# Kernel optimization log

Measured on AMD Instinct MI355X. Metric: run time of the kernel, lower is better.

Reference implementation:

```python
import jax, jax.numpy as jnp
import numpy as np

E = 512
H = 8
D = E // H  # head_dim = 64
SCALE = D ** -0.5
NEG_INF = float('-inf')


def layer_norm(x, g, b, eps=1e-5):
    mu = jnp.mean(x, axis=-1, keepdims=True)
    var = jnp.var(x, axis=-1, keepdims=True)
    return (x - mu) * jax.lax.rsqrt(var + eps) * g + b


def setup_inputs() -> dict:
    key = jax.random.key(0)
    ks = jax.random.split(key, 16)
    B, Q, K = 4, 2048, 2048
    inp = {
        'query': jax.random.normal(ks[0], (B, Q, E), jnp.float32),
        'key_value': jax.random.normal(ks[1], (B, K, E), jnp.float32),
        'kv_mask': jax.random.randint(ks[2], (B, K), 0, 2) > 0,
        'sparse_mask': jax.random.randint(ks[3], (B, Q, K), 0, 2) > 0,
        'ln_q_g': jnp.ones((E,), jnp.float32),
        'ln_q_b': jnp.zeros((E,), jnp.float32),
        'ln_kv_g': jnp.ones((E,), jnp.float32),
        'ln_kv_b': jnp.zeros((E,), jnp.float32),
        # Linear weights stored as (in, out): y = x @ W + b
        'Wq': jax.random.normal(ks[4], (E, E), jnp.float32) * (E ** -0.5),
        'bq': jnp.zeros((E,), jnp.float32),
        'Wk': jax.random.normal(ks[5], (E, E), jnp.float32) * (E ** -0.5),
        'bk': jnp.zeros((E,), jnp.float32),
        'Wv': jax.random.normal(ks[6], (E, E), jnp.float32) * (E ** -0.5),
        'bv': jnp.zeros((E,), jnp.float32),
        'Wo': jax.random.normal(ks[7], (E, E), jnp.float32) * (E ** -0.5),
        'bo': jnp.zeros((E,), jnp.float32),
    }
    return inp


def reference(query, key_value, kv_mask, sparse_mask,
              ln_q_g, ln_q_b, ln_kv_g, ln_kv_b,
              Wq, bq, Wk, bk, Wv, bv, Wo, bo):
    B, Qn, _ = query.shape
    Kn = key_value.shape[1]
    qn = layer_norm(query, ln_q_g, ln_q_b)
    kvn = layer_norm(key_value, ln_kv_g, ln_kv_b)
    q = (qn @ Wq + bq).reshape(B, Qn, H, D)
    k = (kvn @ Wk + bk).reshape(B, Kn, H, D)
    v = (kvn @ Wv + bv).reshape(B, Kn, H, D)
    # scores: [B, H, Q, K]
    scores = jnp.einsum('bqhd,bkhd->bhqk', q, k) * SCALE
    mask = kv_mask[:, None, None, :] & sparse_mask[:, None, :, :]
    scores = jnp.where(mask, scores, NEG_INF)
    attn = jax.nn.softmax(scores, axis=-1)
    # nan_to_num(0): rows with no valid key -> all-zero weights
    valid_row = jnp.any(mask, axis=-1, keepdims=True)
    attn = jnp.where(valid_row, attn, 0.0)
    out = jnp.einsum('bhqk,bkhd->bqhd', attn, v).reshape(B, Qn, E)
    return out @ Wo + bo
```

## Files before the change

### kernel.cpp

```cpp
#include <hip/hip_runtime.h>
#include <hip/hip_bf16.h>
#include <math.h>

typedef unsigned short ushort_t;
typedef __attribute__((ext_vector_type(8))) __bf16 bf16x8;
typedef __attribute__((ext_vector_type(4))) float f32x4;
typedef __attribute__((ext_vector_type(4))) unsigned int u32x4;

#define E_DIM 512
#define HEADS 8
#define HD 64
#define SEQ 2048
#define NROWS 8192
#define QSCALE 0.18033688011112042f

static __device__ __forceinline__ unsigned short f2b(float f) {
  unsigned int x;
  __builtin_memcpy(&x, &f, 4);
  x += 0x7fffu + ((x >> 16) & 1u);
  return (unsigned short)(x >> 16);
}

static __device__ __forceinline__ int swz(int row, int col) {
  return row * 64 + ((((col >> 3) ^ (row & 7)) & 7) << 3) + (col & 7);
}

static __device__ __forceinline__ void gl2lds16(const ushort_t* g, ushort_t* s) {
#if __has_builtin(__builtin_amdgcn_global_load_lds)
  __builtin_amdgcn_global_load_lds(
      (const __attribute__((address_space(1))) unsigned int*)(uintptr_t)g,
      (__attribute__((address_space(3))) unsigned int*)(uintptr_t)s,
      16, 0, 0);
#else
  int l = threadIdx.x & 63;
  *(u32x4*)(s + l * 8) = *(const u32x4*)g;
#endif
}

__launch_bounds__(256)
__global__ void prep_kernel(const float* __restrict__ Wq, const float* __restrict__ Wk,
                            const float* __restrict__ Wv, const float* __restrict__ Wo,
                            ushort_t* __restrict__ WT,
                            const int* __restrict__ kvm, const int* __restrict__ sp,
                            unsigned long long* __restrict__ bits,
                            const float* __restrict__ xq, const float* __restrict__ xkv,
                            const float* __restrict__ gq, const float* __restrict__ bq,
                            const float* __restrict__ gkv, const float* __restrict__ bkv,
                            ushort_t* __restrict__ yq, ushort_t* __restrict__ ykv) {
  int blk = blockIdx.x;
  int t = threadIdx.x;
  if (blk < 1024) {
    int z = blk >> 8, rem = blk & 255;
    const float* in = (z == 0) ? Wq : (z == 1) ? Wk : (z == 2) ? Wv : Wo;
    ushort_t* o = WT + (size_t)z * E_DIM * E_DIM;
    __shared__ float tile[32 * 33];
    int tx = t & 31, ty = t >> 5;
    int n0 = (rem & 15) * 32, k0 = (rem >> 4) * 32;
#pragma unroll
    for (int i = 0; i < 4; ++i) {
      int k = ty + i * 8;
      tile[k * 33 + tx] = in[(k0 + k) * E_DIM + n0 + tx];
    }
    __syncthreads();
#pragma unroll
    for (int i = 0; i < 4; ++i) {
      int n = ty + i * 8;
      o[(n0 + n) * E_DIM + k0 + tx] = f2b(tile[tx * 33 + n]);
    }
  } else if (blk < 3072) {
    int w = t >> 6, l = t & 63;
    int row = (blk - 1024) * 4 + w;
    int b = row >> 11;
    const int* sprow = sp + ((size_t)row << 11);
    const int* kvrow = kvm + (b << 11);
    unsigned long long* out = bits + ((size_t)row << 5);
#pragma unroll 4
    for (int it = 0; it < 32; ++it) {
      int k = it * 64 + l;
      unsigned long long m = __ballot(sprow[k] != 0 && kvrow[k] != 0);
      if (l == 0) out[it] = m;
    }
  } else {
    int idx = blk - 3072;
    int which = idx >> 11;
    const float* x = which ? xkv : xq;
    const float* g = which ? gkv : gq;
    const float* bb = which ? bkv : bq;
    ushort_t* y = which ? ykv : yq;
    int w = t >> 6, l = t & 63;
    int row = (idx & 2047) * 4 + w;
    f32x4 x0 = *(const f32x4*)&x[row * E_DIM + l * 8];
    f32x4 x1 = *(const f32x4*)&x[row * E_DIM + l * 8 + 4];
    float xf[8], s = 0.f, ss = 0.f;
#pragma unroll
    for (int j = 0; j < 8; ++j) {
      xf[j] = (j < 4) ? x0[j] : x1[j - 4];
      s += xf[j];
      ss += xf[j] * xf[j];
    }
#pragma unroll
    for (int off = 32; off > 0; off >>= 1) {
      s += __shfl_xor(s, off);
      ss += __shfl_xor(ss, off);
    }
    float mu = s * (1.f / 512.f);
    float var = fmaxf(ss * (1.f / 512.f) - mu * mu, 0.f);
    float rs = rsqrtf(var + 1e-5f);
    f32x4 g0 = *(const f32x4*)&g[l * 8];
    f32x4 g1 = *(const f32x4*)&g[l * 8 + 4];
    f32x4 b0 = *(const f32x4*)&bb[l * 8];
    f32x4 b1 = *(const f32x4*)&bb[l * 8 + 4];
#pragma unroll
    for (int j = 0; j < 8; ++j) {
      float gv = (j < 4) ? g0[j] : g1[j - 4];
      float bv = (j < 4) ? b0[j] : b1[j - 4];
      y[row * E_DIM + l * 8 + j] = f2b((xf[j] - mu) * rs * gv + bv);
    }
  }
}

__launch_bounds__(256)
__global__ void transposeV(const ushort_t* __restrict__ vp, ushort_t* __restrict__ Vt) {
  __shared__ ushort_t tile[64][72];
  int t = threadIdx.x;
  int k0 = blockIdx.x * 64, h = blockIdx.y, b = blockIdx.z;
#pragma unroll
  for (int it = 0; it < 2; ++it) {
    int row = it * 32 + (t >> 3), col = (t & 7) * 8;
    *(u32x4*)&tile[row][col] =
        *(const u32x4*)&vp[(size_t)(b * SEQ + k0 + row) * E_DIM + h * HD + col];
  }
  __syncthreads();
#pragma unroll
  for (int it = 0; it < 2; ++it) {
    int d = it * 32 + (t >> 3), kc = (t & 7) * 8;
    union { ushort_t u[8]; u32x4 v; } o;
#pragma unroll
    for (int j = 0; j < 8; ++j) o.u[j] = tile[kc + j][d];
    *(u32x4*)&Vt[((size_t)(b * HEADS + h) * HD + d) * SEQ + k0 + kc] = o.v;
  }
}

template <typename OUT_T>
static __device__ __forceinline__ void gemm_core(ushort_t* lA, ushort_t* lB,
                                                 const ushort_t* __restrict__ A,
                                                 const ushort_t* __restrict__ WT,
                                                 const float* __restrict__ bias,
                                                 OUT_T* __restrict__ C, float scale,
                                                 int m0, int n0) {
  int t = threadIdx.x, w = t >> 6, l = t & 63;
  int quad = l >> 4, l15 = l & 15;
  int wm_ = w >> 1, wn_ = w & 1;
  int csrc = ((l & 7) ^ (l >> 3)) * 8;
  int rln = l >> 3;

  f32x4 acc[4][2] = {};
  for (int kk = 0; kk < E_DIM; kk += 64) {
    __syncthreads();
#pragma unroll
    for (int i = 0; i < 4; ++i) {
      int r0 = i * 32 + w * 8;
      gl2lds16(&A[(size_t)(m0 + r0 + rln) * E_DIM + kk + csrc], &lA[r0 * 64]);
    }
#pragma unroll
    for (int i = 0; i < 2; ++i) {
      int r0 = i * 32 + w * 8;
      gl2lds16(&WT[(size_t)(n0 + r0 + rln) * E_DIM + kk + csrc], &lB[r0 * 64]);
    }
    __syncthreads();
#pragma unroll
    for (int ks = 0; ks < 2; ++ks) {
      bf16x8 af[4], bf[2];
#pragma unroll
      for (int mt = 0; mt < 4; ++mt)
        af[mt] = *(const bf16x8*)&lA[swz(wm_ * 64 + mt * 16 + l15, ks * 32 + quad * 8)];
#pragma unroll
      for (int nt = 0; nt < 2; ++nt)
        bf[nt] = *(const bf16x8*)&lB[swz(wn_ * 32 + nt * 16 + l15, ks * 32 + quad * 8)];
#pragma unroll
      for (int mt = 0; mt < 4; ++mt)
#pragma unroll
        for (int nt = 0; nt < 2; ++nt)
          acc[mt][nt] = __builtin_amdgcn_mfma_f32_16x16x32_bf16(af[mt], bf[nt], acc[mt][nt], 0, 0, 0);
    }
  }
#pragma unroll
  for (int nt = 0; nt < 2; ++nt) {
    int col = n0 + wn_ * 32 + nt * 16 + l15;
    float bv = bias[col];
#pragma unroll
    for (int mt = 0; mt < 4; ++mt) {
#pragma unroll
      for (int r = 0; r < 4; ++r) {
        int rowm = m0 + wm_ * 64 + mt * 16 + quad * 4 + r;
        float val = (acc[mt][nt][r] + bv) * scale;
        if constexpr (sizeof(OUT_T) == 2)
          C[rowm * E_DIM + col] = f2b(val);
        else
          C[rowm * E_DIM + col] = val;
      }
    }
  }
}

template <typename OUT_T>
__launch_bounds__(256)
__global__ void gemm_bias(const ushort_t* __restrict__ A, const ushort_t* __restrict__ WT,
                          const float* __restrict__ bias, OUT_T* __restrict__ C, float scale) {
  __shared__ ushort_t lA[128 * 64];
  __shared__ ushort_t lB[64 * 64];
  gemm_core<OUT_T>(lA, lB, A, WT, bias, C, scale, blockIdx.x * 128, blockIdx.y * 64);
}

__launch_bounds__(256)
__global__ void gemm_proj2(const ushort_t* A0, const ushort_t* W0, const float* b0, ushort_t* C0, float s0,
                           const ushort_t* A1, const ushort_t* W1, const float* b1, ushort_t* C1, float s1) {
  __shared__ ushort_t lA[128 * 64];
  __shared__ ushort_t lB[64 * 64];
  int m0 = blockIdx.x * 128, n0 = blockIdx.y * 64;
  if (blockIdx.z == 0) gemm_core<ushort_t>(lA, lB, A0, W0, b0, C0, s0, m0, n0);
  else                 gemm_core<ushort_t>(lA, lB, A1, W1, b1, C1, s1, m0, n0);
}

__launch_bounds__(256)
__global__ void attn_kernel(const ushort_t* __restrict__ Qp, const ushort_t* __restrict__ Kp,
                            const ushort_t* __restrict__ Vt,
                            const unsigned long long* __restrict__ bits,
                            ushort_t* __restrict__ ctx) {
  __shared__ ushort_t sQ[64 * 64];
  __shared__ ushort_t sK[64 * 64];
  __shared__ ushort_t sVt[64 * 64];
  __shared__ ushort_t sP[64 * 64];
  int t = threadIdx.x, w = t >> 6, l = t & 63;
  int quad = l >> 4, l15 = l & 15;
  int q0 = blockIdx.x * 64;
  int h = blockIdx.y;
  int b = blockIdx.z;
  int bh = b * HEADS + h;
  int myq = w * 16 + l15;
  int csrc = ((l & 7) ^ (l >> 3)) * 8;
  int rln = l >> 3;

#pragma unroll
  for (int it = 0; it < 2; ++it) {
    int r0 = it * 32 + w * 8;
    gl2lds16(&Qp[(size_t)(b * SEQ + q0 + r0 + rln) * E_DIM + h * HD + csrc], &sQ[r0 * 64]);
  }

  const unsigned long long* mrow = bits + ((size_t)(b * SEQ + q0 + myq) << 5);
  float lsum = 0.f;
  f32x4 o[4] = {};

  for (int kt = 0; kt < 32; ++kt) {
    int k0 = kt * 64;
    __syncthreads();
#pragma unroll
    for (int it = 0; it < 2; ++it) {
      int r0 = it * 32 + w * 8;
      gl2lds16(&Kp[(size_t)(b * SEQ + k0 + r0 + rln) * E_DIM + h * HD + csrc], &sK[r0 * 64]);
      gl2lds16(&Vt[((size_t)bh * HD + r0 + rln) * SEQ + k0 + csrc], &sVt[r0 * 64]);
    }
    __syncthreads();

    f32x4 s[4] = {};
#pragma unroll
    for (int ks = 0; ks < 2; ++ks) {
      bf16x8 qf = *(const bf16x8*)&sQ[swz(myq, ks * 32 + quad * 8)];
#pragma unroll
      for (int nt = 0; nt < 4; ++nt) {
        bf16x8 kf = *(const bf16x8*)&sK[swz(nt * 16 + l15, ks * 32 + quad * 8)];
        s[nt] = __builtin_amdgcn_mfma_f32_16x16x32_bf16(kf, qf, s[nt], 0, 0, 0);
      }
    }

    unsigned long long wmask = mrow[kt];
    unsigned sx = ((unsigned)wmask) >> (quad * 4);
    unsigned sy = ((unsigned)(wmask >> 32)) >> (quad * 4);
#pragma unroll
    for (int nt = 0; nt < 4; ++nt) {
      unsigned wsel = (nt & 2) ? sy : sx;
      int sh = (nt & 1) ? 16 : 0;
      union { ushort_t u[4]; uint2 v; } pk;
#pragma unroll
      for (int r = 0; r < 4; ++r) {
        float pv = exp2f(s[nt][r]);
        unsigned short uu = (unsigned short)(__float_as_uint(pv) >> 16);
        if (!((wsel >> (sh + r)) & 1u)) uu = 0;
        pk.u[r] = uu;
        lsum += __uint_as_float(((unsigned)uu) << 16);
      }
      *(uint2*)&sP[swz(myq, nt * 16 + quad * 4)] = pk.v;
    }

#pragma unroll
    for (int ks = 0; ks < 2; ++ks) {
      bf16x8 pf = *(const bf16x8*)&sP[swz(myq, ks * 32 + quad * 8)];
#pragma unroll
      for (int mt = 0; mt < 4; ++mt) {
        bf16x8 vf = *(const bf16x8*)&sVt[swz(mt * 16 + l15, ks * 32 + quad * 8)];
        o[mt] = __builtin_amdgcn_mfma_f32_16x16x32_bf16(vf, pf, o[mt], 0, 0, 0);
      }
    }
  }

  lsum += __shfl_xor(lsum, 16);
  lsum += __shfl_xor(lsum, 32);
  float inv = (lsum > 0.f) ? 1.f / lsum : 0.f;
  size_t base = (size_t)(b * SEQ + q0 + myq) * E_DIM + h * HD;
#pragma unroll
  for (int mt = 0; mt < 4; ++mt) {
    union { ushort_t u[4]; uint2 v; } ov;
#pragma unroll
    for (int r = 0; r < 4; ++r) ov.u[r] = f2b(o[mt][r] * inv);
    *(uint2*)&ctx[base + mt * 16 + quad * 4] = ov.v;
  }
}

extern "C" void kernel_launch(void* const* d_in, const int* in_sizes, int n_in,
                              void* d_out, int out_size, void* d_ws, size_t ws_size,
                              hipStream_t stream) {
  const float* query     = (const float*)d_in[0];
  const float* key_value = (const float*)d_in[1];
  const int*   kv_mask   = (const int*)d_in[2];
  const int*   sp_mask   = (const int*)d_in[3];
  const float* ln_q_g  = (const float*)d_in[4];
  const float* ln_q_b  = (const float*)d_in[5];
  const float* ln_kv_g = (const float*)d_in[6];
  const float* ln_kv_b = (const float*)d_in[7];
  const float* Wq = (const float*)d_in[8];
  const float* bq = (const float*)d_in[9];
  const float* Wk = (const float*)d_in[10];
  const float* bk = (const float*)d_in[11];
  const float* Wv = (const float*)d_in[12];
  const float* bv = (const float*)d_in[13];
  const float* Wo = (const float*)d_in[14];
  const float* bo = (const float*)d_in[15];

  const size_t NB = (size_t)NROWS * E_DIM;
  char* ws = (char*)d_ws;
  ushort_t* bufA = (ushort_t*)ws;
  ushort_t* bufB = bufA + NB;
  ushort_t* WT   = bufB + NB;
  ushort_t* WTq = WT;
  ushort_t* WTk = WTq + E_DIM * E_DIM;
  ushort_t* WTv = WTk + E_DIM * E_DIM;
  ushort_t* WTo = WTv + E_DIM * E_DIM;
  unsigned long long* bits = (unsigned long long*)(WTo + E_DIM * E_DIM);

  ushort_t* dlo = (ushort_t*)d_out;
  ushort_t* dhi = dlo + NB;

  prep_kernel<<<7168, 256, 0, stream>>>(Wq, Wk, Wv, Wo, WT, kv_mask, sp_mask, bits,
                                        query, key_value, ln_q_g, ln_q_b, ln_kv_g, ln_kv_b,
                                        dlo, bufA);

  gemm_proj2<<<dim3(64, 8, 2), 256, 0, stream>>>(dlo, WTq, bq, dhi, QSCALE,
                                                 bufA, WTv, bv, bufB, 1.f);

  gemm_bias<ushort_t><<<dim3(64, 8), 256, 0, stream>>>(bufA, WTk, bk, dlo, 1.f);

  transposeV<<<dim3(32, HEADS, 4), 256, 0, stream>>>(bufB, bufA);

  attn_kernel<<<dim3(32, HEADS, 4), 256, 0, stream>>>(dhi, dlo, bufA, bits, bufB);

  gemm_bias<float><<<dim3(64, 8), 256, 0, stream>>>(bufB, WTo, bo, (float*)d_out, 1.f);
}
```

Measured before the change: 295.8 us.

## Fuse V transpose into projection epilogue and widen GEMM tiles to 128x128

The V projection now writes its output directly in the head-transposed layout from the GEMM epilogue, so the separate transposeV kernel and its extra read and write pass are gone. All projection GEMMs move from 128x64 to 128x128 tiles (4x4 MFMA accumulators per wave), which halves the grid and raises data reuse per block. The attention softmax also changes to mask by substituting a large negative value before exp2 and to sum the fp32 probabilities instead of the truncated bf16 ones. The trade-offs are higher register use per thread, fewer blocks to fill the GPU, and strided 8-byte stores in the transposed epilogue.

New measurement: 289.5 us. 2.1% less time.

```diff
diff --git a/kernel.cpp b/kernel.cpp
--- a/kernel.cpp
+++ b/kernel.cpp
@@ -12,6 +12,7 @@
 #define HD 64
 #define SEQ 2048
 #define NROWS 8192
+#define NEGF (-1e30f)
 #define QSCALE 0.18033688011112042f
 
 static __device__ __forceinline__ unsigned short f2b(float f) {
@@ -119,107 +120,103 @@
   }
 }
 
-__launch_bounds__(256)
-__global__ void transposeV(const ushort_t* __restrict__ vp, ushort_t* __restrict__ Vt) {
-  __shared__ ushort_t tile[64][72];
-  int t = threadIdx.x;
-  int k0 = blockIdx.x * 64, h = blockIdx.y, b = blockIdx.z;
-#pragma unroll
-  for (int it = 0; it < 2; ++it) {
-    int row = it * 32 + (t >> 3), col = (t & 7) * 8;
-    *(u32x4*)&tile[row][col] =
-        *(const u32x4*)&vp[(size_t)(b * SEQ + k0 + row) * E_DIM + h * HD + col];
-  }
-  __syncthreads();
-#pragma unroll
-  for (int it = 0; it < 2; ++it) {
-    int d = it * 32 + (t >> 3), kc = (t & 7) * 8;
-    union { ushort_t u[8]; u32x4 v; } o;
-#pragma unroll
-    for (int j = 0; j < 8; ++j) o.u[j] = tile[kc + j][d];
-    *(u32x4*)&Vt[((size_t)(b * HEADS + h) * HD + d) * SEQ + k0 + kc] = o.v;
-  }
-}
-
-template <typename OUT_T>
-static __device__ __forceinline__ void gemm_core(ushort_t* lA, ushort_t* lB,
-                                                 const ushort_t* __restrict__ A,
-                                                 const ushort_t* __restrict__ WT,
-                                                 const float* __restrict__ bias,
-                                                 OUT_T* __restrict__ C, float scale,
-                                                 int m0, int n0) {
+template <int MODE>
+static __device__ __forceinline__ void gemm_core128(ushort_t* lA, ushort_t* lB,
+                                                    const ushort_t* __restrict__ A,
+                                                    const ushort_t* __restrict__ WT,
+                                                    const float* __restrict__ bias,
+                                                    void* Cv, float scale, int m0, int n0) {
   int t = threadIdx.x, w = t >> 6, l = t & 63;
   int quad = l >> 4, l15 = l & 15;
   int wm_ = w >> 1, wn_ = w & 1;
   int csrc = ((l & 7) ^ (l >> 3)) * 8;
   int rln = l >> 3;
 
-  f32x4 acc[4][2] = {};
+  f32x4 acc[4][4] = {};
   for (int kk = 0; kk < E_DIM; kk += 64) {
     __syncthreads();
 #pragma unroll
     for (int i = 0; i < 4; ++i) {
       int r0 = i * 32 + w * 8;
       gl2lds16(&A[(size_t)(m0 + r0 + rln) * E_DIM + kk + csrc], &lA[r0 * 64]);
-    }
-#pragma unroll
-    for (int i = 0; i < 2; ++i) {
-      int r0 = i * 32 + w * 8;
       gl2lds16(&WT[(size_t)(n0 + r0 + rln) * E_DIM + kk + csrc], &lB[r0 * 64]);
     }
     __syncthreads();
 #pragma unroll
     for (int ks = 0; ks < 2; ++ks) {
-      bf16x8 af[4], bf[2];
+      bf16x8 af[4], bf[4];
 #pragma unroll
       for (int mt = 0; mt < 4; ++mt)
         af[mt] = *(const bf16x8*)&lA[swz(wm_ * 64 + mt * 16 + l15, ks * 32 + quad * 8)];
 #pragma unroll
-      for (int nt = 0; nt < 2; ++nt)
-        bf[nt] = *(const bf16x8*)&lB[swz(wn_ * 32 + nt * 16 + l15, ks * 32 + quad * 8)];
+      for (int nt = 0; nt < 4; ++nt)
+        bf[nt] = *(const bf16x8*)&lB[swz(wn_ * 64 + nt * 16 + l15, ks * 32 + quad * 8)];
 #pragma unroll
       for (int mt = 0; mt < 4; ++mt)
 #pragma unroll
-        for (int nt = 0; nt < 2; ++nt)
+        for (int nt = 0; nt < 4; ++nt)
           acc[mt][nt] = __builtin_amdgcn_mfma_f32_16x16x32_bf16(af[mt], bf[nt], acc[mt][nt], 0, 0, 0);
     }
   }
-#pragma unroll
-  for (int nt = 0; nt < 2; ++nt) {
-    int col = n0 + wn_ * 32 + nt * 16 + l15;
+
+#pragma unroll
+  for (int nt = 0; nt < 4; ++nt) {
+    int col = n0 + wn_ * 64 + nt * 16 + l15;
     float bv = bias[col];
-#pragma unroll
-    for (int mt = 0; mt < 4; ++mt) {
-#pragma unroll
-      for (int r = 0; r < 4; ++r) {
-        int rowm = m0 + wm_ * 64 + mt * 16 + quad * 4 + r;
-        float val = (acc[mt][nt][r] + bv) * scale;
-        if constexpr (sizeof(OUT_T) == 2)
-          C[rowm * E_DIM + col] = f2b(val);
-        else
-          C[rowm * E_DIM + col] = val;
-      }
-    }
-  }
-}
-
-template <typename OUT_T>
-__launch_bounds__(256)
-__global__ void gemm_bias(const ushort_t* __restrict__ A, const ushort_t* __restrict__ WT,
-                          const float* __restrict__ bias, OUT_T* __restrict__ C, float scale) {
+    if constexpr (MODE == 2) {
+      int h = col >> 6, d = col & 63;
+#pragma unroll
+      for (int mt = 0; mt < 4; ++mt) {
+        int row = m0 + wm_ * 64 + mt * 16 + quad * 4;
+        int b = row >> 11, k = row & 2047;
+        union { ushort_t u[4]; uint2 v; } pk;
+#pragma unroll
+        for (int r = 0; r < 4; ++r) pk.u[r] = f2b(acc[mt][nt][r] + bv);
+        *(uint2*)&((ushort_t*)Cv)[((((size_t)(b * HEADS + h)) * HD + d) << 11) + k] = pk.v;
+      }
+    } else {
+#pragma unroll
+      for (int mt = 0; mt < 4; ++mt) {
+#pragma unroll
+        for (int r = 0; r < 4; ++r) {
+          int rowm = m0 + wm_ * 64 + mt * 16 + quad * 4 + r;
+          float val = (acc[mt][nt][r] + bv) * scale;
+          if constexpr (MODE == 0)
+            ((ushort_t*)Cv)[rowm * E_DIM + col] = f2b(val);
+          else
+            ((float*)Cv)[rowm * E_DIM + col] = val;
+        }
+      }
+    }
+  }
+}
+
+__launch_bounds__(256)
+__global__ void gemm128_bf16(const ushort_t* __restrict__ A, const ushort_t* __restrict__ WT,
+                             const float* __restrict__ bias, ushort_t* __restrict__ C, float scale) {
   __shared__ ushort_t lA[128 * 64];
-  __shared__ ushort_t lB[64 * 64];
-  gemm_core<OUT_T>(lA, lB, A, WT, bias, C, scale, blockIdx.x * 128, blockIdx.y * 64);
-}
-
-__launch_bounds__(256)
-__global__ void gemm_proj2(const ushort_t* A0, const ushort_t* W0, const float* b0, ushort_t* C0, float s0,
-                           const ushort_t* A1, const ushort_t* W1, const float* b1, ushort_t* C1, float s1) {
+  __shared__ ushort_t lB[128 * 64];
+  gemm_core128<0>(lA, lB, A, WT, bias, C, scale, blockIdx.x * 128, blockIdx.y * 128);
+}
+
+__launch_bounds__(256)
+__global__ void gemm128_f32(const ushort_t* __restrict__ A, const ushort_t* __restrict__ WT,
+                            const float* __restrict__ bias, float* __restrict__ C) {
   __shared__ ushort_t lA[128 * 64];
-  __shared__ ushort_t lB[64 * 64];
-  int m0 = blockIdx.x * 128, n0 = blockIdx.y * 64;
-  if (blockIdx.z == 0) gemm_core<ushort_t>(lA, lB, A0, W0, b0, C0, s0, m0, n0);
-  else                 gemm_core<ushort_t>(lA, lB, A1, W1, b1, C1, s1, m0, n0);
+  __shared__ ushort_t lB[128 * 64];
+  gemm_core128<1>(lA, lB, A, WT, bias, C, 1.f, blockIdx.x * 128, blockIdx.y * 128);
+}
+
+__launch_bounds__(256)
+__global__ void proj2_kernel(const ushort_t* __restrict__ qn, const ushort_t* __restrict__ WTq,
+                             const float* __restrict__ bq, ushort_t* __restrict__ qp,
+                             const ushort_t* __restrict__ kvn, const ushort_t* __restrict__ WTv,
+                             const float* __restrict__ bv, ushort_t* __restrict__ Vt) {
+  __shared__ ushort_t lA[128 * 64];
+  __shared__ ushort_t lB[128 * 64];
+  int m0 = blockIdx.x * 128, n0 = blockIdx.y * 128;
+  if (blockIdx.z == 0) gemm_core128<0>(lA, lB, qn, WTq, bq, qp, QSCALE, m0, n0);
+  else                 gemm_core128<2>(lA, lB, kvn, WTv, bv, Vt, 1.f, m0, n0);
 }
 
 __launch_bounds__(256)
@@ -283,11 +280,10 @@
       union { ushort_t u[4]; uint2 v; } pk;
 #pragma unroll
       for (int r = 0; r < 4; ++r) {
-        float pv = exp2f(s[nt][r]);
-        unsigned short uu = (unsigned short)(__float_as_uint(pv) >> 16);
-        if (!((wsel >> (sh + r)) & 1u)) uu = 0;
-        pk.u[r] = uu;
-        lsum += __uint_as_float(((unsigned)uu) << 16);
+        float smv = ((wsel >> (sh + r)) & 1u) ? s[nt][r] : NEGF;
+        float pv = exp2f(smv);
+        pk.u[r] = (unsigned short)(__float_as_uint(pv) >> 16);
+        lsum += pv;
       }
       *(uint2*)&sP[swz(myq, nt * 16 + quad * 4)] = pk.v;
     }
@@ -354,14 +350,12 @@
                                         query, key_value, ln_q_g, ln_q_b, ln_kv_g, ln_kv_b,
                                         dlo, bufA);
 
-  gemm_proj2<<<dim3(64, 8, 2), 256, 0, stream>>>(dlo, WTq, bq, dhi, QSCALE,
-                                                 bufA, WTv, bv, bufB, 1.f);
-
-  gemm_bias<ushort_t><<<dim3(64, 8), 256, 0, stream>>>(bufA, WTk, bk, dlo, 1.f);
-
-  transposeV<<<dim3(32, HEADS, 4), 256, 0, stream>>>(bufB, bufA);
-
-  attn_kernel<<<dim3(32, HEADS, 4), 256, 0, stream>>>(dhi, dlo, bufA, bits, bufB);
-
-  gemm_bias<float><<<dim3(64, 8), 256, 0, stream>>>(bufB, WTo, bo, (float*)d_out, 1.f);
-}
+  proj2_kernel<<<dim3(64, 4, 2), 256, 0, stream>>>(dlo, WTq, bq, dhi,
+                                                   bufA, WTv, bv, bufB);
+
+  gemm128_bf16<<<dim3(64, 4), 256, 0, stream>>>(bufA, WTk, bk, dlo, 1.f);
+
+  attn_kernel<<<dim3(32, HEADS, 4), 256, 0, stream>>>(dhi, dlo, bufB, bits, bufA);
+
+  gemm128_f32<<<dim3(64, 4), 256, 0, stream>>>(bufA, WTo, bo, (float*)d_out);
+}
```
